# Kernel tuning notes

Hardware: AMD Instinct MI355X
Metric: run time of the kernel (lower is better)

Reference implementation:

```python
import jax, jax.numpy as jnp
import numpy as np

N_NODES = 10000
N_EDGES = 160000
IN_CH = 256
HIDDEN = 512
N_LAYERS = 2
W_SCALE = 0.05  # keep relu chain numerically tame


def setup_inputs() -> dict:
    key = jax.random.key(0)
    ks = jax.random.split(key, 8)
    x = jax.random.normal(ks[0], (N_NODES, IN_CH), dtype=jnp.float32)
    edge_index = jax.random.randint(ks[1], (2, N_EDGES), 0, N_NODES, dtype=jnp.int64)
    W_in = jax.random.normal(ks[2], (IN_CH, HIDDEN), dtype=jnp.float32) * W_SCALE
    b_in = jnp.zeros((HIDDEN,), jnp.float32)
    msg_W = jax.random.normal(ks[3], (N_LAYERS, HIDDEN, HIDDEN), dtype=jnp.float32) * W_SCALE
    msg_b = jnp.zeros((N_LAYERS, HIDDEN), jnp.float32)
    upd_W = jax.random.normal(ks[4], (N_LAYERS, 2 * HIDDEN, HIDDEN), dtype=jnp.float32) * W_SCALE
    upd_b = jnp.zeros((N_LAYERS, HIDDEN), jnp.float32)
    W_out = jax.random.normal(ks[5], (HIDDEN, 1), dtype=jnp.float32) * W_SCALE
    b_out = jnp.zeros((1,), jnp.float32)
    return {"x": x, "edge_index": edge_index, "W_in": W_in, "b_in": b_in,
            "msg_W": msg_W, "msg_b": msg_b, "upd_W": upd_W, "upd_b": upd_b,
            "W_out": W_out, "b_out": b_out}


def reference(x, edge_index, W_in, b_in, msg_W, msg_b, upd_W, upd_b, W_out, b_out):
    src = edge_index[0]  # x_j source nodes (PyG source_to_target flow)
    dst = edge_index[1]  # aggregate into destination nodes
    n = x.shape[0]
    h = jax.nn.relu(x @ W_in + b_in)  # [N, H]
    for l in range(msg_W.shape[0]):
        # message: relu(Linear(x_j)) on gathered source features  [E, H]
        m = jax.nn.relu(h[src] @ msg_W[l] + msg_b[l])
        # aggr='add': scatter-add over destination nodes  [N, H]
        aggr = jax.ops.segment_sum(m, dst, num_segments=n)
        # update: relu(Linear(concat([x, aggr])))  [N, H]
        h = jax.nn.relu(jnp.concatenate([h, aggr], axis=-1) @ upd_W[l] + upd_b[l])
    out = h @ W_out + b_out  # [N, 1]
    return out.squeeze(-1)
```

## Files before the change

### kernel.cpp

```cpp
#include <hip/hip_runtime.h>


typedef _Float16 half8 __attribute__((ext_vector_type(8)));
typedef float float4v __attribute__((ext_vector_type(4)));

#define ASYNC_COPY16(gptr, lptr)                                              \
    __builtin_amdgcn_global_load_lds(                                         \
        (const __attribute__((address_space(1))) void*)(gptr),                \
        (__attribute__((address_space(3))) void*)(lptr), 16, 0, 0)


__device__ __forceinline__ void gemm_body(int id,
    const _Float16* __restrict__ A1, int KT1,
    const _Float16* __restrict__ A2, int KT2,
    const _Float16* __restrict__ Wt, int KTw, int ktw2,
    const float* __restrict__ bias, _Float16* __restrict__ C,
    int M, int Mtiles, int packC, int do_relu,
    const float* __restrict__ Wout, const float* __restrict__ bout,
    float* __restrict__ outp)
{
    __shared__ _Float16 As[8192];
    __shared__ _Float16 Bs[4096];

    const int tid  = threadIdx.x;
    const int wave = tid >> 6, lane = tid & 63;

    const int cxcd = id & 7, j = id >> 3;
    const int mt = cxcd + 8 * (j >> 3);
    if (mt >= Mtiles) return;
    const int pn = j & 7;
    const int bm = mt * 128, bn = pn * 64;

    const int wr  = wave * 32;
    const int m16 = lane & 15, quad = lane >> 4;
    const int sub = wave >> 1;
    const int rb  = (wave & 1) * 32;

    float4v acc[2][4] = {};
    float bv[4];
    #pragma unroll
    for (int jj = 0; jj < 4; ++jj) bv[jj] = bias[bn + jj * 16 + m16];

    for (int pass = 0; pass < 2; ++pass) {
        const _Float16* __restrict__ A = pass ? A2 : A1;
        if (A == nullptr) continue;
        const int KTa  = pass ? KT2 : KT1;
        const int ktw0 = pass ? ktw2 : 0;

        for (int kt = 0; kt < KTa; ++kt) {
            const _Float16* Ab0 = A + (size_t)((2 * mt)     * KTa + kt) * 4096;
            const _Float16* Ab1 = A + (size_t)((2 * mt + 1) * KTa + kt) * 4096;
            const _Float16* Wb  = Wt + (size_t)(pn * KTw + ktw0 + kt) * 4096;
            #pragma unroll
            for (int t = 0; t < 2; ++t) {
                const int q = t * 4 + wave;
                ASYNC_COPY16(Ab0 + q * 512 + lane * 8, (char*)As + q * 1024);
                ASYNC_COPY16(Ab1 + q * 512 + lane * 8, (char*)As + 8192 + q * 1024);
                ASYNC_COPY16(Wb  + q * 512 + lane * 8, (char*)Bs + q * 1024);
            }
            __syncthreads();
            #pragma unroll
            for (int c = 0; c < 2; ++c) {
                const int ch = c * 4 + quad;
                half8 af[2], bf[4];
                #pragma unroll
                for (int i2 = 0; i2 < 2; ++i2)
                    af[i2] = *(const half8*)
                        &As[sub * 4096 + (ch * 64 + ((rb + i2 * 16 + m16) ^ ch)) * 8];
                #pragma unroll
                for (int j2 = 0; j2 < 4; ++j2)
                    bf[j2] = *(const half8*)
                        &Bs[(ch * 64 + ((j2 * 16 + m16) ^ ch)) * 8];
                #pragma unroll
                for (int i2 = 0; i2 < 2; ++i2)
                    #pragma unroll
                    for (int j2 = 0; j2 < 4; ++j2)
                        acc[i2][j2] = __builtin_amdgcn_mfma_f32_16x16x32_f16(
                            af[i2], bf[j2], acc[i2][j2], 0, 0, 0);
            }
            __syncthreads();
        }
    }

    if (outp) {
        #pragma unroll
        for (int i = 0; i < 2; ++i)
            #pragma unroll
            for (int rg = 0; rg < 4; ++rg) {
                const int r2 = wr + i * 16 + quad * 4 + rg;
                const int row = bm + r2;
                float pr = 0.f;
                #pragma unroll
                for (int j2 = 0; j2 < 4; ++j2) {
                    float v = fmaxf(acc[i][j2][rg] + bv[j2], 0.f);
                    pr += v * Wout[bn + j2 * 16 + m16];
                }
                pr += __shfl_xor(pr, 1);
                pr += __shfl_xor(pr, 2);
                pr += __shfl_xor(pr, 4);
                pr += __shfl_xor(pr, 8);
                if (m16 == 0 && row < M)
                    atomicAdd(&outp[row], pr + (pn == 0 ? bout[0] : 0.f));
            }
        return;
    }

    #pragma unroll
    for (int i = 0; i < 2; ++i)
        #pragma unroll
        for (int rg = 0; rg < 4; ++rg) {
            const int r2 = wr + i * 16 + quad * 4 + rg;
            const int row = bm + r2;
            #pragma unroll
            for (int j2 = 0; j2 < 4; ++j2) {
                float v = acc[i][j2][rg] + bv[j2];
                if (do_relu) v = fmaxf(v, 0.f);
                const int coff = j2 * 16 + m16;
                if (packC) {
                    C[(size_t)(((mt * 2 + (r2 >> 6)) * 8 + pn) * 8 + (coff >> 3)) * 512
                      + ((r2 & 63) ^ (coff >> 3)) * 8 + (coff & 7)] = (_Float16)v;
                } else {
                    C[(size_t)row * 512 + bn + coff] = (_Float16)v;
                }
            }
        }
}

__global__ __launch_bounds__(256) void gemm_f16(
    const _Float16* __restrict__ A1, int KT1,
    const _Float16* __restrict__ A2, int KT2,
    const _Float16* __restrict__ Wt, int KTw, int ktw2,
    const float* __restrict__ bias, _Float16* __restrict__ C,
    int M, int Mtiles, int packC, int do_relu,
    const float* Wout, const float* bout, float* outp)
{
    gemm_body(blockIdx.x, A1, KT1, A2, KT2, Wt, KTw, ktw2,
              bias, C, M, Mtiles, packC, do_relu, Wout, bout, outp);
}

__device__ __forceinline__ void transpose_unit(
    const float* __restrict__ src, _Float16* __restrict__ dst, int R, int tb)
{
    const int rtiles = R >> 5;
    const int r0 = (tb % rtiles) * 32, c0 = (tb / rtiles) * 32;
    const int KT = R >> 6;
    __shared__ float t[32][33];
    const int tid = threadIdx.x;
    const int tx = tid & 31, ty = tid >> 5;
    #pragma unroll
    for (int i = 0; i < 32; i += 8)
        t[ty + i][tx] = src[(size_t)(r0 + ty + i) * 512 + c0 + tx];
    __syncthreads();
    if (tid < 128) {
        const int n  = c0 + (tid >> 2);
        const int k0 = r0 + (tid & 3) * 8;
        half8 o;
        #pragma unroll
        for (int j2 = 0; j2 < 8; ++j2)
            o[j2] = (_Float16)t[(tid & 3) * 8 + j2][tid >> 2];
        *(half8*)&dst[(size_t)(((n >> 6) * KT + (k0 >> 6)) * 8 + ((k0 >> 3) & 7)) * 512
                      + ((n & 63) ^ ((k0 >> 3) & 7)) * 8] = o;
    }
}

__global__ __launch_bounds__(256) void fill_ingemm(
    const int* __restrict__ eidx, int* __restrict__ cursor,
    int* __restrict__ srcs, int E,
    const _Float16* __restrict__ xb, const _Float16* __restrict__ WinT,
    const float* __restrict__ b_in, _Float16* __restrict__ B0,
    int M, int Mtiles,
    const float* __restrict__ msg_W, _Float16* __restrict__ msgT,
    const float* __restrict__ upd_W, _Float16* __restrict__ updT)
{
    const int gemmU = ((Mtiles + 7) >> 3) * 64;
    const int fillU = (E + 255) >> 8;
    const int b = blockIdx.x;
    if (b < gemmU) {
        gemm_body(b, xb, 4, nullptr, 0, WinT, 4, 0,
                  b_in, B0, M, Mtiles, 1, 1, nullptr, nullptr, nullptr);
        return;
    }
    if (b < gemmU + fillU) {
        const int e = (b - gemmU) * 256 + threadIdx.x;
        if (e < E) {
            const int d = eidx[E + e];
            const int pos = atomicAdd(&cursor[d], 1);
            if (pos < 64) srcs[d * 64 + pos] = eidx[e];
        }
        return;
    }
    const int tB = b - gemmU - fillU;
    if (tB < 256)       transpose_unit(msg_W,              msgT,              512,  tB);
    else if (tB < 512)  transpose_unit(msg_W + 512 * 512,  msgT + 512 * 512,  512,  tB - 256);
    else if (tB < 1024) transpose_unit(upd_W,              updT,              1024, tB - 512);
    else                transpose_unit(upd_W + 1024 * 512, updT + 512 * 1024, 1024, tB - 1024);
}

__global__ __launch_bounds__(256) void prep(
    const float* __restrict__ W_in,  _Float16* __restrict__ WinT,
    const float* __restrict__ x,     _Float16* __restrict__ xb,
    int* __restrict__ cursor, float* __restrict__ outz,
    int n4, int M)
{
    const int b = blockIdx.x;
    const int tid = threadIdx.x;
    const int castU = (n4 + 255) >> 8;
    if (b < 128) {
        transpose_unit(W_in, WinT, 256, b);
    } else if (b < 128 + castU) {
        const int i = (b - 128) * 256 + tid;
        if (i < n4) {
            const float4 v = *(const float4*)(x + (size_t)i * 4);
            ushort4 s;
            union { _Float16 h; unsigned short u; } cv;
            cv.h = (_Float16)v.x; s.x = cv.u;
            cv.h = (_Float16)v.y; s.y = cv.u;
            cv.h = (_Float16)v.z; s.z = cv.u;
            cv.h = (_Float16)v.w; s.w = cv.u;
            const int f = i * 4;
            const int m = f >> 8, k = f & 255;
            *(ushort4*)((unsigned short*)xb
                + (size_t)(((m >> 6) * 4 + (k >> 6)) * 8 + ((k >> 3) & 7)) * 512
                + ((m & 63) ^ ((k >> 3) & 7)) * 8 + (k & 7)) = s;
        }
    } else {
        const int zi = (b - 128 - castU) * 256 + tid;
        if (zi < M) { cursor[zi] = 0; outz[zi] = 0.f; }
    }
}

__global__ __launch_bounds__(256) void aggregate_f16(
    const _Float16* __restrict__ hmr, const int* __restrict__ cursor,
    const int* __restrict__ srcs, _Float16* __restrict__ ag, int n)
{
    const int l16  = threadIdx.x & 15;
    const int node = blockIdx.x * 16 + (threadIdx.x >> 4);
    if (node >= n) return;
    const int c8 = blockIdx.y * 128 + l16 * 8;
    const int beg = node * 64;
    const int end = beg + min(cursor[node], 64);
    float a[8] = {};
    int j = beg;
    for (; j + 3 < end; j += 4) {
        const half8 v0 = *(const half8*)(hmr + (size_t)srcs[j]     * 512 + c8);
        const half8 v1 = *(const half8*)(hmr + (size_t)srcs[j + 1] * 512 + c8);
        const half8 v2 = *(const half8*)(hmr + (size_t)srcs[j + 2] * 512 + c8);
        const half8 v3 = *(const half8*)(hmr + (size_t)srcs[j + 3] * 512 + c8);
        #pragma unroll
        for (int i = 0; i < 8; ++i)
            a[i] += ((float)v0[i] + (float)v1[i]) + ((float)v2[i] + (float)v3[i]);
    }
    for (; j < end; ++j) {
        const half8 v = *(const half8*)(hmr + (size_t)srcs[j] * 512 + c8);
        #pragma unroll
        for (int i = 0; i < 8; ++i) a[i] += (float)v[i];
    }
    half8 o;
    #pragma unroll
    for (int i = 0; i < 8; ++i) o[i] = (_Float16)a[i];
    *(half8*)(ag + (size_t)(((node >> 6) * 8 + (c8 >> 6)) * 8 + ((c8 >> 3) & 7)) * 512
              + ((node & 63) ^ ((c8 >> 3) & 7)) * 8) = o;
}

extern "C" void kernel_launch(void* const* d_in, const int* in_sizes, int n_in,
                              void* d_out, int out_size, void* d_ws, size_t ws_size,
                              hipStream_t stream)
{
    const float* x     = (const float*)d_in[0];
    const int*   eidx  = (const int*)  d_in[1];
    const float* W_in  = (const float*)d_in[2];
    const float* b_in  = (const float*)d_in[3];
    const float* msg_W = (const float*)d_in[4];
    const float* msg_b = (const float*)d_in[5];
    const float* upd_W = (const float*)d_in[6];
    const float* upd_b = (const float*)d_in[7];
    const float* W_out = (const float*)d_in[8];
    const float* b_out = (const float*)d_in[9];

    const int IN = 256, H = 512;
    const int M = in_sizes[0] / IN;
    const int E = in_sizes[1] / 2;
    const int Mtiles = (M + 127) / 128;
    const size_t Mt = (size_t)Mtiles * 128;

    _Float16* xb   = (_Float16*)d_ws;
    _Float16* B0   = xb + Mt * IN;
    _Float16* B1   = B0 + Mt * H;
    _Float16* B2   = B1 + Mt * H;
    _Float16* WinT = B2 + Mt * H;
    _Float16* msgT = WinT + (size_t)H * IN;
    _Float16* updT = msgT + (size_t)2 * H * H;
    int* cursor = (int*)(updT + (size_t)2 * H * 2 * H);
    int* srcs   = cursor + M;

    const dim3 blk(256);
    const int gemmBlocks = ((Mtiles + 7) / 8) * 64;
    const dim3 aggrGrid((M + 15) / 16, 4);

    const int n4 = M * IN / 4;
    const int castU = (n4 + 255) / 256;
    const int fillU = (E + 255) / 256;
    const int zeroU = (M + 255) / 256;
    const int transU = 1536;

    prep<<<dim3(128 + castU + zeroU), blk, 0, stream>>>(
        W_in, WinT, x, xb, cursor, (float*)d_out, n4, M);
    fill_ingemm<<<dim3(gemmBlocks + fillU + transU), blk, 0, stream>>>(
        eidx, cursor, srcs, E, xb, WinT, b_in, B0, M, Mtiles,
        msg_W, msgT, upd_W, updT);

    gemm_f16<<<dim3(gemmBlocks), blk, 0, stream>>>(B0, 8, nullptr, 0,
        msgT, 8, 0, msg_b, B1, M, Mtiles, 0, 1,
        nullptr, nullptr, nullptr);
    aggregate_f16<<<aggrGrid, blk, 0, stream>>>(B1, cursor, srcs, B2, M);
    gemm_f16<<<dim3(gemmBlocks), blk, 0, stream>>>(B0, 8, B2, 8,
        updT, 16, 8, upd_b, B1, M, Mtiles, 1, 1,
        nullptr, nullptr, nullptr);
    gemm_f16<<<dim3(gemmBlocks), blk, 0, stream>>>(B1, 8, nullptr, 0,
        msgT + 512 * 512, 8, 0, msg_b + 512, B0, M, Mtiles, 0, 1,
        nullptr, nullptr, nullptr);
    aggregate_f16<<<aggrGrid, blk, 0, stream>>>(B0, cursor, srcs, B2, M);
    gemm_f16<<<dim3(gemmBlocks), blk, 0, stream>>>(B1, 8, B2, 8,
        updT + 512 * 1024, 16, 8, upd_b + 512, nullptr, M, Mtiles, 1, 1,
        W_out, b_out, (float*)d_out);
}
```

Before: 204.7 us.

## Double-buffer LDS tiles in GEMM to overlap async loads with MFMA

```diff
diff --git a/kernel.cpp b/kernel.cpp
--- a/kernel.cpp
+++ b/kernel.cpp
@@ -19,8 +19,8 @@
     const float* __restrict__ Wout, const float* __restrict__ bout,
     float* __restrict__ outp)
 {
-    __shared__ _Float16 As[8192];
-    __shared__ _Float16 Bs[4096];
+    __shared__ _Float16 As[16384];
+    __shared__ _Float16 Bs[8192];
 
     const int tid  = threadIdx.x;
     const int wave = tid >> 6, lane = tid & 63;
@@ -41,45 +41,62 @@
     #pragma unroll
     for (int jj = 0; jj < 4; ++jj) bv[jj] = bias[bn + jj * 16 + m16];
 
-    for (int pass = 0; pass < 2; ++pass) {
-        const _Float16* __restrict__ A = pass ? A2 : A1;
-        if (A == nullptr) continue;
-        const int KTa  = pass ? KT2 : KT1;
-        const int ktw0 = pass ? ktw2 : 0;
-
-        for (int kt = 0; kt < KTa; ++kt) {
-            const _Float16* Ab0 = A + (size_t)((2 * mt)     * KTa + kt) * 4096;
-            const _Float16* Ab1 = A + (size_t)((2 * mt + 1) * KTa + kt) * 4096;
-            const _Float16* Wb  = Wt + (size_t)(pn * KTw + ktw0 + kt) * 4096;
-            #pragma unroll
-            for (int t = 0; t < 2; ++t) {
-                const int q = t * 4 + wave;
-                ASYNC_COPY16(Ab0 + q * 512 + lane * 8, (char*)As + q * 1024);
-                ASYNC_COPY16(Ab1 + q * 512 + lane * 8, (char*)As + 8192 + q * 1024);
-                ASYNC_COPY16(Wb  + q * 512 + lane * 8, (char*)Bs + q * 1024);
-            }
-            __syncthreads();
-            #pragma unroll
-            for (int c = 0; c < 2; ++c) {
-                const int ch = c * 4 + quad;
-                half8 af[2], bf[4];
-                #pragma unroll
-                for (int i2 = 0; i2 < 2; ++i2)
-                    af[i2] = *(const half8*)
-                        &As[sub * 4096 + (ch * 64 + ((rb + i2 * 16 + m16) ^ ch)) * 8];
+    const int total = KT1 + (A2 ? KT2 : 0);
+
+    auto stageT = [&](int t, int BUF) {
+        const _Float16* __restrict__ A;
+        int KTa, kt;
+        if (t < KT1) { A = A1; KTa = KT1; kt = t; }
+        else         { A = A2; KTa = KT2; kt = t - KT1; }
+        const int ktw = (t < KT1) ? t : ktw2 + (t - KT1);
+        const _Float16* Ab0 = A  + (size_t)((2 * mt)     * KTa + kt) * 4096;
+        const _Float16* Ab1 = A  + (size_t)((2 * mt + 1) * KTa + kt) * 4096;
+        const _Float16* Wb  = Wt + (size_t)(pn * KTw + ktw) * 4096;
+        #pragma unroll
+        for (int t2 = 0; t2 < 2; ++t2) {
+            const int q = t2 * 4 + wave;
+            ASYNC_COPY16(Ab0 + q * 512 + lane * 8,
+                         (char*)As + BUF * 16384 + q * 1024);
+            ASYNC_COPY16(Ab1 + q * 512 + lane * 8,
+                         (char*)As + BUF * 16384 + 8192 + q * 1024);
+            ASYNC_COPY16(Wb  + q * 512 + lane * 8,
+                         (char*)Bs + BUF * 8192 + q * 1024);
+        }
+    };
+
+    auto computeT = [&](int BUF) {
+        #pragma unroll
+        for (int c = 0; c < 2; ++c) {
+            const int ch = c * 4 + quad;
+            half8 af[2], bf[4];
+            #pragma unroll
+            for (int i2 = 0; i2 < 2; ++i2)
+                af[i2] = *(const half8*)
+                    &As[BUF * 8192 + sub * 4096
+                        + (ch * 64 + ((rb + i2 * 16 + m16) ^ ch)) * 8];
+            #pragma unroll
+            for (int j2 = 0; j2 < 4; ++j2)
+                bf[j2] = *(const half8*)
+                    &Bs[BUF * 4096 + (ch * 64 + ((j2 * 16 + m16) ^ ch)) * 8];
+            #pragma unroll
+            for (int i2 = 0; i2 < 2; ++i2)
                 #pragma unroll
                 for (int j2 = 0; j2 < 4; ++j2)
-                    bf[j2] = *(const half8*)
-                        &Bs[(ch * 64 + ((j2 * 16 + m16) ^ ch)) * 8];
-                #pragma unroll
-                for (int i2 = 0; i2 < 2; ++i2)
-                    #pragma unroll
-                    for (int j2 = 0; j2 < 4; ++j2)
-                        acc[i2][j2] = __builtin_amdgcn_mfma_f32_16x16x32_f16(
-                            af[i2], bf[j2], acc[i2][j2], 0, 0, 0);
-            }
-            __syncthreads();
-        }
+                    acc[i2][j2] = __builtin_amdgcn_mfma_f32_16x16x32_f16(
+                        af[i2], bf[j2], acc[i2][j2], 0, 0, 0);
+        }
+    };
+
+    stageT(0, 0);
+    __syncthreads();
+    for (int t = 0; t < total; t += 2) {
+        if (t + 1 < total) stageT(t + 1, 1);
+        computeT(0);
+        __syncthreads();
+        if (t + 1 >= total) break;
+        if (t + 2 < total) stageT(t + 2, 0);
+        computeT(1);
+        __syncthreads();
     }
 
     if (outp) {
```

Result: slower. 239.1 us (+16.8%).
